# Optimization experiments

Measured on AMD Instinct MI355X. Metric: run time of the kernel, lower is better.

The kernel has to match this reference:

```python
import jax, jax.numpy as jnp
import numpy as np

EMBEDDING_DIM = 100
M = 50                      # chunk width
NUM_CHUNK = EMBEDDING_DIM // M  # 2
VOCAB = 100000
EPS = 1e-8                  # torch CosineSimilarity eps


def setup_inputs() -> dict:
    key = jax.random.key(0)
    k_idx, k_emb, k_w, k_u = jax.random.split(key, 4)
    word_idxs = jax.random.randint(k_idx, (4096, 200), 0, VOCAB)  # [B, L]
    # embedding table initialized uniform(-1, 1) as in the original np.random.uniform
    emb_table = jax.random.uniform(k_emb, (VOCAB, EMBEDDING_DIM), dtype=jnp.float32,
                                   minval=-1.0, maxval=1.0)
    weights = jnp.ones((EMBEDDING_DIM, 1), dtype=jnp.float32)      # output projection
    attend_u = jnp.ones((NUM_CHUNK, M), dtype=jnp.float32)         # per-chunk attention query
    return {"word_idxs": word_idxs, "emb_table": emb_table,
            "weights": weights, "attend_u": attend_u}


def reference(word_idxs, emb_table, weights, attend_u):
    B, L = word_idxs.shape
    embeds = emb_table[word_idxs]                       # [B, L, 100]
    ch = embeds.reshape(B, L, NUM_CHUNK, M)             # [B, L, C, M]
    # cosine similarity per word vs per-chunk query (torch eps semantics)
    e_norm = ch / jnp.maximum(jnp.linalg.norm(ch, axis=-1, keepdims=True), EPS)
    u_norm = attend_u / jnp.maximum(jnp.linalg.norm(attend_u, axis=-1, keepdims=True), EPS)
    cos = jnp.einsum('blcm,cm->blc', e_norm, u_norm)    # [B, L, C]
    alphas = jnp.exp(cos)                               # positive -> L1 norm == sum
    norm_alphas = alphas / jnp.sum(alphas, axis=1, keepdims=True)
    hidden = jnp.einsum('blcm,blc->bcm', ch, norm_alphas).reshape(B, EMBEDDING_DIM)
    return hidden @ weights                             # [B, 1]
```

## Files before the change

### kernel.cpp

```cpp
#include <hip/hip_runtime.h>

constexpr int C_ = 2;
constexpr int M_ = 50;
constexpr int ED = 100;
constexpr float EPS = 1e-8f;


__global__ __launch_bounds__(256) void row_stats_kernel(
    const float* __restrict__ emb,
    const float* __restrict__ wgt,
    const float* __restrict__ att,
    float*       __restrict__ tbl,
    int vocab)
{
    __shared__ float2 s_uw[ED];
    __shared__ float  s_su[C_];

    const int t = threadIdx.x;
    if (t < ED) s_uw[t] = make_float2(att[t], wgt[t]);
    __syncthreads();
    if (t < C_) {
        float ss = 0.f;
        #pragma unroll
        for (int m = 0; m < M_; ++m) { float v = s_uw[t * M_ + m].x; ss += v * v; }
        s_su[t] = 1.0f / fmaxf(sqrtf(ss), EPS);
    }
    __syncthreads();

    const int wave = t >> 6;
    const int lane = t & 63;
    const int g    = lane >> 2;
    const int j    = lane & 3;
    const int r    = blockIdx.x * 64 + wave * 16 + g;
    if (r >= vocab) return;

    const float4* rowp = reinterpret_cast<const float4*>(emb + (long long)r * ED);

    float sq0 = 0.f, du0 = 0.f, dw0 = 0.f;
    float sq1 = 0.f, du1 = 0.f, dw1 = 0.f;

    #pragma unroll
    for (int it = 0; it < 6; ++it) {
        const float4 v = rowp[4 * it + j];
        const float xs[4] = { v.x, v.y, v.z, v.w };
        #pragma unroll
        for (int k = 0; k < 4; ++k) {
            const int ebase = 16 * it + k;
            const float x   = xs[k];
            const float2 uw = s_uw[ebase + 4 * j];
            if (ebase + 12 < M_) {
                sq0 = fmaf(x, x, sq0); du0 = fmaf(x, uw.x, du0); dw0 = fmaf(x, uw.y, dw0);
            } else if (ebase >= M_) {
                sq1 = fmaf(x, x, sq1); du1 = fmaf(x, uw.x, du1); dw1 = fmaf(x, uw.y, dw1);
            } else {
                if (j == 0) { sq0 = fmaf(x, x, sq0); du0 = fmaf(x, uw.x, du0); dw0 = fmaf(x, uw.y, dw0); }
                else        { sq1 = fmaf(x, x, sq1); du1 = fmaf(x, uw.x, du1); dw1 = fmaf(x, uw.y, dw1); }
            }
        }
    }
    if (j == 0) {
        const float4 v = rowp[24];
        const float xs[4] = { v.x, v.y, v.z, v.w };
        #pragma unroll
        for (int k = 0; k < 4; ++k) {
            const float2 uw = s_uw[96 + k];
            sq1 = fmaf(xs[k], xs[k], sq1); du1 = fmaf(xs[k], uw.x, du1); dw1 = fmaf(xs[k], uw.y, dw1);
        }
    }

    #pragma unroll
    for (int m = 1; m < 4; m <<= 1) {
        sq0 += __shfl_xor(sq0, m, 4);
        du0 += __shfl_xor(du0, m, 4);
        dw0 += __shfl_xor(dw0, m, 4);
        sq1 += __shfl_xor(sq1, m, 4);
        du1 += __shfl_xor(du1, m, 4);
        dw1 += __shfl_xor(dw1, m, 4);
    }

    if (j == 0) {
        const float cos0 = du0 / fmaxf(sqrtf(sq0), EPS) * s_su[0];
        const float cos1 = du1 / fmaxf(sqrtf(sq1), EPS) * s_su[1];
        const float a0 = __expf(cos0);
        const float a1 = __expf(cos1);
        reinterpret_cast<float4*>(tbl)[r] = make_float4(a0, a0 * dw0, a1, a1 * dw1);
    }
}

__global__ __launch_bounds__(256) void attend_kernel(
    const int*    __restrict__ idx,
    const float4* __restrict__ tbl,
    float*        __restrict__ out,
    int B, int L)
{
    __shared__ float4 s_part[4];

    const int half = threadIdx.x >> 7;
    const int tt   = threadIdx.x & 127;
    const int b    = blockIdx.x * 2 + half;

    float a0 = 0.f, ap0 = 0.f, a1 = 0.f, ap1 = 0.f;
    if (b < B) {
        const int* ib = idx + (long long)b * L;
        #pragma unroll 2
        for (int l = tt; l < L; l += 128) {
            const float4 v = tbl[ib[l]];
            a0 += v.x; ap0 += v.y; a1 += v.z; ap1 += v.w;
        }
        #pragma unroll
        for (int off = 32; off > 0; off >>= 1) {
            a0  += __shfl_down(a0,  off, 64);
            a1  += __shfl_down(a1,  off, 64);
            ap0 += __shfl_down(ap0, off, 64);
            ap1 += __shfl_down(ap1, off, 64);
        }
    }

    const int wave = threadIdx.x >> 6;
    if ((threadIdx.x & 63) == 0) s_part[wave] = make_float4(a0, ap0, a1, ap1);
    __syncthreads();

    if (tt == 0 && b < B) {
        const float4 p = s_part[half * 2];
        const float4 q = s_part[half * 2 + 1];
        out[b] = (p.y + q.y) / (p.x + q.x) + (p.w + q.w) / (p.z + q.z);
    }
}

extern "C" void kernel_launch(void* const* d_in, const int* in_sizes, int n_in,
                              void* d_out, int out_size, void* d_ws, size_t ws_size,
                              hipStream_t stream) {
    const int*   idx = (const int*)d_in[0];
    const float* emb = (const float*)d_in[1];
    const float* wgt = (const float*)d_in[2];
    const float* att = (const float*)d_in[3];
    float* out = (float*)d_out;

    const int B     = out_size;
    const int L     = in_sizes[0] / B;
    const int vocab = in_sizes[1] / ED;

    float* tbl = (float*)d_ws;

    row_stats_kernel<<<(vocab + 63) / 64, 256, 0, stream>>>(emb, wgt, att, tbl, vocab);
    attend_kernel<<<(B + 1) / 2, 256, 0, stream>>>(idx, (const float4*)tbl, out, B, L);
}
```

Before: 92.54 us.

## Fuse row-stats and attend kernels with a software grid barrier

Merges the two launches into one persistent kernel. Blocks grid-stride over vocab row groups to build the per-row table, then meet at a global barrier built from atomic slots with hash-tagged values, and each wave then reduces one batch row. Index loads for the gather are issued before the barrier to hide latency. This removes one kernel launch and the gap between kernels, but it depends on all 1024 blocks being co-resident (a deadlock risk otherwise) and on slot values left over from earlier calls not matching by chance. Those stale values could let blocks pass the barrier before the table is fully written.

```diff
diff --git a/kernel.cpp b/kernel.cpp
--- a/kernel.cpp
+++ b/kernel.cpp
@@ -6,12 +6,20 @@
 constexpr float EPS = 1e-8f;
 
 
-__global__ __launch_bounds__(256) void row_stats_kernel(
+__device__ __forceinline__ unsigned long long slot_val(unsigned i) {
+    const unsigned lo = (i + 1u) * 2654435761u;
+    return ((unsigned long long)(~lo) << 32) | (unsigned long long)lo;
+}
+
+__global__ __launch_bounds__(256, 4) void fused_kernel(
+    const int*   __restrict__ idx,
     const float* __restrict__ emb,
     const float* __restrict__ wgt,
     const float* __restrict__ att,
+    float*       __restrict__ out,
     float*       __restrict__ tbl,
-    int vocab)
+    unsigned long long* __restrict__ slots,
+    int B, int L, int vocab, int nblk)
 {
     __shared__ float2 s_uw[ED];
     __shared__ float  s_su[C_];
@@ -27,84 +35,118 @@
     }
     __syncthreads();
 
-    const int wave = t >> 6;
+    const int wv   = t >> 6;
     const int lane = t & 63;
     const int g    = lane >> 2;
     const int j    = lane & 3;
-    const int r    = blockIdx.x * 64 + wave * 16 + g;
-    if (r >= vocab) return;
-
-    const float4* rowp = reinterpret_cast<const float4*>(emb + (long long)r * ED);
-
-    float sq0 = 0.f, du0 = 0.f, dw0 = 0.f;
-    float sq1 = 0.f, du1 = 0.f, dw1 = 0.f;
-
-    #pragma unroll
-    for (int it = 0; it < 6; ++it) {
-        const float4 v = rowp[4 * it + j];
-        const float xs[4] = { v.x, v.y, v.z, v.w };
-        #pragma unroll
-        for (int k = 0; k < 4; ++k) {
-            const int ebase = 16 * it + k;
-            const float x   = xs[k];
-            const float2 uw = s_uw[ebase + 4 * j];
-            if (ebase + 12 < M_) {
-                sq0 = fmaf(x, x, sq0); du0 = fmaf(x, uw.x, du0); dw0 = fmaf(x, uw.y, dw0);
-            } else if (ebase >= M_) {
-                sq1 = fmaf(x, x, sq1); du1 = fmaf(x, uw.x, du1); dw1 = fmaf(x, uw.y, dw1);
-            } else {
-                if (j == 0) { sq0 = fmaf(x, x, sq0); du0 = fmaf(x, uw.x, du0); dw0 = fmaf(x, uw.y, dw0); }
-                else        { sq1 = fmaf(x, x, sq1); du1 = fmaf(x, uw.x, du1); dw1 = fmaf(x, uw.y, dw1); }
-            }
-        }
-    }
-    if (j == 0) {
-        const float4 v = rowp[24];
-        const float xs[4] = { v.x, v.y, v.z, v.w };
-        #pragma unroll
-        for (int k = 0; k < 4; ++k) {
-            const float2 uw = s_uw[96 + k];
-            sq1 = fmaf(xs[k], xs[k], sq1); du1 = fmaf(xs[k], uw.x, du1); dw1 = fmaf(xs[k], uw.y, dw1);
-        }
-    }
-
-    #pragma unroll
-    for (int m = 1; m < 4; m <<= 1) {
-        sq0 += __shfl_xor(sq0, m, 4);
-        du0 += __shfl_xor(du0, m, 4);
-        dw0 += __shfl_xor(dw0, m, 4);
-        sq1 += __shfl_xor(sq1, m, 4);
-        du1 += __shfl_xor(du1, m, 4);
-        dw1 += __shfl_xor(dw1, m, 4);
-    }
-
-    if (j == 0) {
-        const float cos0 = du0 / fmaxf(sqrtf(sq0), EPS) * s_su[0];
-        const float cos1 = du1 / fmaxf(sqrtf(sq1), EPS) * s_su[1];
-        const float a0 = __expf(cos0);
-        const float a1 = __expf(cos1);
-        reinterpret_cast<float4*>(tbl)[r] = make_float4(a0, a0 * dw0, a1, a1 * dw1);
-    }
-}
-
-__global__ __launch_bounds__(256) void attend_kernel(
-    const int*    __restrict__ idx,
-    const float4* __restrict__ tbl,
-    float*        __restrict__ out,
-    int B, int L)
-{
-    __shared__ float4 s_part[4];
-
-    const int half = threadIdx.x >> 7;
-    const int tt   = threadIdx.x & 127;
-    const int b    = blockIdx.x * 2 + half;
-
-    float a0 = 0.f, ap0 = 0.f, a1 = 0.f, ap1 = 0.f;
-    if (b < B) {
-        const int* ib = idx + (long long)b * L;
-        #pragma unroll 2
-        for (int l = tt; l < L; l += 128) {
-            const float4 v = tbl[ib[l]];
+
+    const int ngroups = (vocab + 15) >> 4;
+    const int NW      = nblk * 4;
+    for (int task = blockIdx.x * 4 + wv; task < ngroups; task += NW) {
+        const int r = task * 16 + g;
+        if (r < vocab) {
+            const float4* rowp = reinterpret_cast<const float4*>(emb + (long long)r * ED);
+
+            float sq0 = 0.f, du0 = 0.f, dw0 = 0.f;
+            float sq1 = 0.f, du1 = 0.f, dw1 = 0.f;
+
+            #pragma unroll
+            for (int it = 0; it < 6; ++it) {
+                const float4 v = rowp[4 * it + j];
+                const float xs[4] = { v.x, v.y, v.z, v.w };
+                #pragma unroll
+                for (int k = 0; k < 4; ++k) {
+                    const int ebase = 16 * it + k;
+                    const float x   = xs[k];
+                    const float2 uw = s_uw[ebase + 4 * j];
+                    if (ebase + 12 < M_) {
+                        sq0 = fmaf(x, x, sq0); du0 = fmaf(x, uw.x, du0); dw0 = fmaf(x, uw.y, dw0);
+                    } else if (ebase >= M_) {
+                        sq1 = fmaf(x, x, sq1); du1 = fmaf(x, uw.x, du1); dw1 = fmaf(x, uw.y, dw1);
+                    } else {
+                        if (j == 0) { sq0 = fmaf(x, x, sq0); du0 = fmaf(x, uw.x, du0); dw0 = fmaf(x, uw.y, dw0); }
+                        else        { sq1 = fmaf(x, x, sq1); du1 = fmaf(x, uw.x, du1); dw1 = fmaf(x, uw.y, dw1); }
+                    }
+                }
+            }
+            if (j == 0) {
+                const float4 v = rowp[24];
+                const float xs[4] = { v.x, v.y, v.z, v.w };
+                #pragma unroll
+                for (int k = 0; k < 4; ++k) {
+                    const float2 uw = s_uw[96 + k];
+                    sq1 = fmaf(xs[k], xs[k], sq1); du1 = fmaf(xs[k], uw.x, du1); dw1 = fmaf(xs[k], uw.y, dw1);
+                }
+            }
+
+            #pragma unroll
+            for (int m = 1; m < 4; m <<= 1) {
+                sq0 += __shfl_xor(sq0, m, 4); du0 += __shfl_xor(du0, m, 4); dw0 += __shfl_xor(dw0, m, 4);
+                sq1 += __shfl_xor(sq1, m, 4); du1 += __shfl_xor(du1, m, 4); dw1 += __shfl_xor(dw1, m, 4);
+            }
+
+            if (j == 0) {
+                const float cos0 = du0 / fmaxf(sqrtf(sq0), EPS) * s_su[0];
+                const float cos1 = du1 / fmaxf(sqrtf(sq1), EPS) * s_su[1];
+                const float a0 = __expf(cos0);
+                const float a1 = __expf(cos1);
+                reinterpret_cast<float4*>(tbl)[r] = make_float4(a0, a0 * dw0, a1, a1 * dw1);
+            }
+        }
+    }
+
+    const int  b      = blockIdx.x * 4 + wv;
+    const bool bvalid = (b < B);
+    const int* ib     = idx + (long long)b * L;
+    int pre[4];
+    #pragma unroll
+    for (int m = 0; m < 4; ++m) {
+        const int l = lane + 64 * m;
+        pre[m] = (bvalid && l < L) ? ib[l] : 0;
+    }
+
+    __threadfence();
+    __syncthreads();
+    if (t == 0) {
+        __hip_atomic_store(&slots[blockIdx.x], slot_val(blockIdx.x),
+                           __ATOMIC_RELEASE, __HIP_MEMORY_SCOPE_AGENT);
+    }
+    if (blockIdx.x == 0) {
+        for (int s = t; s < nblk; s += 256) {
+            const unsigned long long want = slot_val((unsigned)s);
+            while (__hip_atomic_load(&slots[s], __ATOMIC_ACQUIRE,
+                                     __HIP_MEMORY_SCOPE_AGENT) != want)
+                __builtin_amdgcn_s_sleep(8);
+        }
+        __syncthreads();
+        if (t == 0) {
+            __threadfence();
+            __hip_atomic_store(&slots[nblk], slot_val(0x40000000u),
+                               __ATOMIC_RELEASE, __HIP_MEMORY_SCOPE_AGENT);
+        }
+    }
+    if (t == 0) {
+        const unsigned long long wantgo = slot_val(0x40000000u);
+        while (__hip_atomic_load(&slots[nblk], __ATOMIC_ACQUIRE,
+                                 __HIP_MEMORY_SCOPE_AGENT) != wantgo)
+            __builtin_amdgcn_s_sleep(32);
+    }
+    __syncthreads();
+    __threadfence();
+
+    if (bvalid) {
+        float a0 = 0.f, ap0 = 0.f, a1 = 0.f, ap1 = 0.f;
+        const float4* tb4 = reinterpret_cast<const float4*>(tbl);
+        #pragma unroll
+        for (int m = 0; m < 4; ++m) {
+            const int l = lane + 64 * m;
+            if (l < L) {
+                const float4 v = tb4[pre[m]];
+                a0 += v.x; ap0 += v.y; a1 += v.z; ap1 += v.w;
+            }
+        }
+        for (int l = lane + 256; l < L; l += 64) {
+            const float4 v = tb4[ib[l]];
             a0 += v.x; ap0 += v.y; a1 += v.z; ap1 += v.w;
         }
         #pragma unroll
@@ -114,17 +156,87 @@
             ap0 += __shfl_down(ap0, off, 64);
             ap1 += __shfl_down(ap1, off, 64);
         }
-    }
-
-    const int wave = threadIdx.x >> 6;
-    if ((threadIdx.x & 63) == 0) s_part[wave] = make_float4(a0, ap0, a1, ap1);
-    __syncthreads();
-
-    if (tt == 0 && b < B) {
-        const float4 p = s_part[half * 2];
-        const float4 q = s_part[half * 2 + 1];
-        out[b] = (p.y + q.y) / (p.x + q.x) + (p.w + q.w) / (p.z + q.z);
-    }
+        if (lane == 0) out[b] = ap0 / a0 + ap1 / a1;
+    }
+}
+
+__global__ __launch_bounds__(256) void row_stats_kernel(
+    const float* __restrict__ emb, const float* __restrict__ wgt,
+    const float* __restrict__ att, float* __restrict__ tbl, int vocab)
+{
+    __shared__ float2 s_uw[ED];
+    __shared__ float  s_su[C_];
+    const int t = threadIdx.x;
+    if (t < ED) s_uw[t] = make_float2(att[t], wgt[t]);
+    __syncthreads();
+    if (t < C_) {
+        float ss = 0.f;
+        #pragma unroll
+        for (int m = 0; m < M_; ++m) { float v = s_uw[t * M_ + m].x; ss += v * v; }
+        s_su[t] = 1.0f / fmaxf(sqrtf(ss), EPS);
+    }
+    __syncthreads();
+    const int wave = t >> 6, lane = t & 63, g = lane >> 2, j = lane & 3;
+    const int r = blockIdx.x * 64 + wave * 16 + g;
+    if (r >= vocab) return;
+    const float4* rowp = reinterpret_cast<const float4*>(emb + (long long)r * ED);
+    float sq0 = 0.f, du0 = 0.f, dw0 = 0.f, sq1 = 0.f, du1 = 0.f, dw1 = 0.f;
+    #pragma unroll
+    for (int it = 0; it < 6; ++it) {
+        const float4 v = rowp[4 * it + j];
+        const float xs[4] = { v.x, v.y, v.z, v.w };
+        #pragma unroll
+        for (int k = 0; k < 4; ++k) {
+            const int ebase = 16 * it + k;
+            const float x = xs[k];
+            const float2 uw = s_uw[ebase + 4 * j];
+            if (ebase + 12 < M_)      { sq0 = fmaf(x,x,sq0); du0 = fmaf(x,uw.x,du0); dw0 = fmaf(x,uw.y,dw0); }
+            else if (ebase >= M_)     { sq1 = fmaf(x,x,sq1); du1 = fmaf(x,uw.x,du1); dw1 = fmaf(x,uw.y,dw1); }
+            else if (j == 0)          { sq0 = fmaf(x,x,sq0); du0 = fmaf(x,uw.x,du0); dw0 = fmaf(x,uw.y,dw0); }
+            else                      { sq1 = fmaf(x,x,sq1); du1 = fmaf(x,uw.x,du1); dw1 = fmaf(x,uw.y,dw1); }
+        }
+    }
+    if (j == 0) {
+        const float4 v = rowp[24];
+        const float xs[4] = { v.x, v.y, v.z, v.w };
+        #pragma unroll
+        for (int k = 0; k < 4; ++k) {
+            const float2 uw = s_uw[96 + k];
+            sq1 = fmaf(xs[k],xs[k],sq1); du1 = fmaf(xs[k],uw.x,du1); dw1 = fmaf(xs[k],uw.y,dw1);
+        }
+    }
+    #pragma unroll
+    for (int m = 1; m < 4; m <<= 1) {
+        sq0 += __shfl_xor(sq0,m,4); du0 += __shfl_xor(du0,m,4); dw0 += __shfl_xor(dw0,m,4);
+        sq1 += __shfl_xor(sq1,m,4); du1 += __shfl_xor(du1,m,4); dw1 += __shfl_xor(dw1,m,4);
+    }
+    if (j == 0) {
+        const float cos0 = du0 / fmaxf(sqrtf(sq0), EPS) * s_su[0];
+        const float cos1 = du1 / fmaxf(sqrtf(sq1), EPS) * s_su[1];
+        const float a0 = __expf(cos0), a1 = __expf(cos1);
+        reinterpret_cast<float4*>(tbl)[r] = make_float4(a0, a0 * dw0, a1, a1 * dw1);
+    }
+}
+
+__global__ __launch_bounds__(256) void attend_kernel(
+    const int* __restrict__ idx, const float4* __restrict__ tbl,
+    float* __restrict__ out, int B, int L)
+{
+    const int wave = threadIdx.x >> 6, lane = threadIdx.x & 63;
+    const int b = blockIdx.x * 4 + wave;
+    if (b >= B) return;
+    const int* ib = idx + (long long)b * L;
+    float a0 = 0.f, a1 = 0.f, ap0 = 0.f, ap1 = 0.f;
+    for (int l = lane; l < L; l += 64) {
+        const float4 v = tbl[ib[l]];
+        a0 += v.x; ap0 += v.y; a1 += v.z; ap1 += v.w;
+    }
+    #pragma unroll
+    for (int off = 32; off > 0; off >>= 1) {
+        a0 += __shfl_down(a0,off,64); a1 += __shfl_down(a1,off,64);
+        ap0 += __shfl_down(ap0,off,64); ap1 += __shfl_down(ap1,off,64);
+    }
+    if (lane == 0) out[b] = ap0 / a0 + ap1 / a1;
 }
 
 extern "C" void kernel_launch(void* const* d_in, const int* in_sizes, int n_in,
@@ -141,7 +253,16 @@
     const int vocab = in_sizes[1] / ED;
 
     float* tbl = (float*)d_ws;
-
-    row_stats_kernel<<<(vocab + 63) / 64, 256, 0, stream>>>(emb, wgt, att, tbl, vocab);
-    attend_kernel<<<(B + 1) / 2, 256, 0, stream>>>(idx, (const float4*)tbl, out, B, L);
-}
+    const int nblk = (B + 3) / 4;
+
+    if (nblk <= 1024 && ws_size >= (size_t)vocab * 16 + 4096 + (size_t)(nblk + 1) * 8) {
+        const size_t slot_off = ((size_t)vocab * 16 + 255) & ~(size_t)255;
+        unsigned long long* slots =
+            (unsigned long long*)((char*)d_ws + slot_off);
+        fused_kernel<<<nblk, 256, 0, stream>>>(idx, emb, wgt, att, out,
+                                               tbl, slots, B, L, vocab, nblk);
+    } else {
+        row_stats_kernel<<<(vocab + 63) / 64, 256, 0, stream>>>(emb, wgt, att, tbl, vocab);
+        attend_kernel<<<(B + 3) / 4, 256, 0, stream>>>(idx, (const float4*)tbl, out, B, L);
+    }
+}
```

Result: slower. 318.6 us (+244.3%).
